# Kernel tuning notes

Measured on AMD Instinct MI355X. Metric: run time of the kernel, lower is better.

## Reference

```python
import jax, jax.numpy as jnp
import numpy as np

N, E, H, ED, TD = 10000, 320000, 128, 64, 32

def _lin(x, w, b):
    return x @ w + b

def _ln(x, g, b, eps=1e-5):
    m = jnp.mean(x, axis=-1, keepdims=True)
    v = jnp.var(x, axis=-1, keepdims=True)
    return (x - m) * jax.lax.rsqrt(v + eps) * g + b

def _mlp(x, w1, b1, g, bt, w2, b2):
    y = jax.nn.silu(_ln(_lin(x, w1, b1), g, bt))
    return _lin(y, w2, b2)

def setup_inputs() -> dict:
    key = jax.random.key(0)
    ks = jax.random.split(key, 32)
    s = 0.02
    nrm = lambda k, shp: jax.random.normal(k, shp, jnp.float32) * s
    d = {}
    d['h'] = jax.random.normal(ks[0], (N, H), jnp.float32)
    d['edge_attr'] = jax.random.normal(ks[1], (E, ED), jnp.float32)
    d['edge_time_emb'] = jax.random.normal(ks[2], (E, TD), jnp.float32)
    d['edge_index'] = jax.random.randint(ks[3], (2, E), 0, N)
    # edge_emb + edge_norm
    d['w_ee'] = nrm(ks[4], (ED + TD, ED)); d['b_ee'] = jnp.zeros((ED,), jnp.float32)
    d['g_en'] = jnp.ones((ED + TD,), jnp.float32); d['bt_en'] = jnp.zeros((ED + TD,), jnp.float32)
    # node_linear / bond_linear
    d['w_nl'] = nrm(ks[5], (H, H)); d['b_nl'] = jnp.zeros((H,), jnp.float32)
    d['w_bl'] = nrm(ks[6], (ED, H)); d['b_bl'] = jnp.zeros((H,), jnp.float32)
    # bond_linear_left/right, node_linear_left/right
    d['w_bll'] = nrm(ks[7], (ED, H)); d['b_bll'] = jnp.zeros((H,), jnp.float32)
    d['w_blr'] = nrm(ks[8], (ED, H)); d['b_blr'] = jnp.zeros((H,), jnp.float32)
    d['w_nll'] = nrm(ks[9], (H, H)); d['b_nll'] = jnp.zeros((H,), jnp.float32)
    d['w_nlr'] = nrm(ks[10], (H, H)); d['b_nlr'] = jnp.zeros((H,), jnp.float32)
    # left / right MLPs: Linear(2H,H), LayerNorm(H), SiLU, Linear(H,H)
    d['mlpl_w1'] = nrm(ks[11], (2 * H, H)); d['mlpl_b1'] = jnp.zeros((H,), jnp.float32)
    d['mlpl_g'] = jnp.ones((H,), jnp.float32); d['mlpl_bt'] = jnp.zeros((H,), jnp.float32)
    d['mlpl_w2'] = nrm(ks[12], (H, H)); d['mlpl_b2'] = jnp.zeros((H,), jnp.float32)
    d['mlpr_w1'] = nrm(ks[13], (2 * H, H)); d['mlpr_b1'] = jnp.zeros((H,), jnp.float32)
    d['mlpr_g'] = jnp.ones((H,), jnp.float32); d['mlpr_bt'] = jnp.zeros((H,), jnp.float32)
    d['mlpr_w2'] = nrm(ks[14], (H, H)); d['mlpr_b2'] = jnp.zeros((H,), jnp.float32)
    # layer_norm(3H) + bond_out: Linear(3H,H), SiLU, Linear(H,ED)
    d['g_ln'] = jnp.ones((3 * H,), jnp.float32); d['bt_ln'] = jnp.zeros((3 * H,), jnp.float32)
    d['w_o1'] = nrm(ks[15], (3 * H, H)); d['b_o1'] = jnp.zeros((H,), jnp.float32)
    d['w_o2'] = nrm(ks[16], (H, ED)); d['b_o2'] = jnp.zeros((ED,), jnp.float32)
    return d

def reference(h, edge_attr, edge_time_emb, edge_index,
              w_ee, b_ee, g_en, bt_en, w_nl, b_nl, w_bl, b_bl,
              w_bll, b_bll, w_blr, b_blr, w_nll, b_nll, w_nlr, b_nlr,
              mlpl_w1, mlpl_b1, mlpl_g, mlpl_bt, mlpl_w2, mlpl_b2,
              mlpr_w1, mlpr_b1, mlpr_g, mlpr_bt, mlpr_w2, mlpr_b2,
              g_ln, bt_ln, w_o1, b_o1, w_o2, b_o2):
    src, dst = edge_index[0], edge_index[1]
    n = h.shape[0]
    # edge_attr = edge_emb(edge_norm(cat([edge_attr, edge_time_emb])))
    ea = _lin(_ln(jnp.concatenate([edge_attr, edge_time_emb], axis=-1), g_en, bt_en), w_ee, b_ee)
    # node linears applied per-node then gathered (same math as gather-then-linear)
    x_i = _lin(h, w_nll, b_nll)[src]            # [E, H]
    x_j = _lin(h, w_nlr, b_nlr)[dst]            # [E, H]
    edge_i = _lin(ea, w_bll, b_bll)             # [E, H]
    edge_j = _lin(ea, w_blr, b_blr)             # [E, H]
    inter_i = _mlp(jnp.concatenate([edge_i, x_i], axis=-1), mlpl_w1, mlpl_b1, mlpl_g, mlpl_bt, mlpl_w2, mlpl_b2)
    inter_j = _mlp(jnp.concatenate([edge_j, x_j], axis=-1), mlpr_w1, mlpr_b1, mlpr_g, mlpr_bt, mlpr_w2, mlpr_b2)
    # scatter_sum to nodes, then regather on the same index
    inter_i = jax.ops.segment_sum(inter_i, src, num_segments=n)[src]
    inter_j = jax.ops.segment_sum(inter_j, dst, num_segments=n)[dst]
    h_node = _lin(h, w_nl, b_nl)
    h_bond = jnp.concatenate([inter_i + inter_j, h_node[src] + h_node[dst], _lin(ea, w_bl, b_bl)], axis=-1)  # [E, 3H]
    h_bond = _ln(h_bond, g_ln, bt_ln)
    out = _lin(jax.nn.silu(_lin(h_bond, w_o1, b_o1)), w_o2, b_o2)  # [E, ED]
    return out
```

## Files before the change

kernel.cpp:

```cpp
#include <hip/hip_runtime.h>
#include <math.h>


using u16 = unsigned short;
using u32 = unsigned int;
typedef __attribute__((ext_vector_type(8))) short  short8;
typedef __attribute__((ext_vector_type(4))) float  f32x4;
typedef __attribute__((ext_vector_type(4))) u32    uint4v;
typedef __attribute__((ext_vector_type(2))) u32    uint2v;

constexpr int NN = 10000;
constexpr int EE = 320000;
constexpr int MAXDEG = 96;

__device__ __forceinline__ float b2f(u16 v) {
  return __builtin_bit_cast(float, (u32)v << 16);
}
__device__ __forceinline__ float b2f_lo(u32 v) {
  return __builtin_bit_cast(float, v << 16);
}
__device__ __forceinline__ float b2f_hi(u32 v) {
  return __builtin_bit_cast(float, v & 0xffff0000u);
}
__device__ __forceinline__ u32 cvtpk(float lo, float hi) {
  u32 r;
  asm("v_cvt_pk_bf16_f32 %0, %1, %2" : "=v"(r) : "v"(lo), "v"(hi));
  return r;
}
__device__ __forceinline__ u16 f2b(float f) {
  return (u16)cvtpk(f, f);
}
__device__ __forceinline__ uint2v pack4(f32x4 v) {
  uint2v r;
  r.x = cvtpk(v[0], v[1]);
  r.y = cvtpk(v[2], v[3]);
  return r;
}
__device__ __forceinline__ u32 addpk(u32 a, u32 b) {
  return cvtpk(b2f_lo(a) + b2f_lo(b), b2f_hi(a) + b2f_hi(b));
}
__device__ __forceinline__ float silu_f(float v) {
  return v * __builtin_amdgcn_rcpf(1.f + __expf(-v));
}

struct Params {
  const void* h; const void* edge_attr; const void* te;
  const int* eidx;
  const int* flag;
  const u16 *b_ee, *g_en, *bt_en;
  const u16 *b_nl, *b_bl, *b_bll, *b_blr, *b_nll, *b_nlr;
  const u16 *l_b1, *l_g, *l_bt, *l_b2;
  const u16 *r_b1, *r_g, *r_bt, *r_b2;
  const u16 *g_ln, *bt_ln, *b_o1, *b_o2;
  const u16 *w_eeT, *w_blT, *w_bllT, *w_blrT, *w_nlT, *w_nllT, *w_nlrT;
  const u16 *l_w1T, *l_w2T, *r_w1T, *r_w2T, *o1T, *o2T;
  u16 *a_nll, *a_nlr, *h_node, *ea_ws;
  u32 *cnt0, *cnt1, *elist0, *elist1;
  u16 *accb_i, *accb_j;
  float *accf_i, *accf_j;
  u16 *inter0, *inter1;
  int amode;
  void *out;
};

__global__ __launch_bounds__(256) void k_sniff(const u16* p, int* flag)
{
  __shared__ int c;
  if (threadIdx.x == 0) c = 0;
  __syncthreads();
  u16 v = p[threadIdx.x * 2];
  int e = (v >> 7) & 0xff;
  if (e >= 100 && e <= 140) atomicAdd(&c, 1);
  __syncthreads();
  if (threadIdx.x == 0) *flag = (c >= 200) ? 1 : 0;
}

template<int K, int CT, int RT>
__device__ __forceinline__ void wave_gemm(const u16* A, int SA,
                                          const u16* __restrict__ BT,
                                          f32x4 (&acc)[RT][CT], int n0)
{
  const int lane = threadIdx.x & 63;
  const int quad = lane >> 4, l16 = lane & 15;
  constexpr int NKT = K / 32;
  short8 b[CT], bn[CT], a[RT], an[RT];
  const int k0 = quad * 8;
#pragma unroll
  for (int c = 0; c < CT; ++c)
    b[c] = *(const short8*)(BT + (size_t)(n0 + c * 16 + l16) * K + k0);
#pragma unroll
  for (int rt = 0; rt < RT; ++rt)
    a[rt] = *(const short8*)(A + (rt * 16 + l16) * SA + k0);
#pragma unroll
  for (int kt = 0; kt < NKT; ++kt) {
    if (kt + 1 < NKT) {
      const int k1 = (kt + 1) * 32 + quad * 8;
#pragma unroll
      for (int c = 0; c < CT; ++c)
        bn[c] = *(const short8*)(BT + (size_t)(n0 + c * 16 + l16) * K + k1);
#pragma unroll
      for (int rt = 0; rt < RT; ++rt)
        an[rt] = *(const short8*)(A + (rt * 16 + l16) * SA + k1);
    }
#pragma unroll
    for (int rt = 0; rt < RT; ++rt)
#pragma unroll
      for (int c = 0; c < CT; ++c)
        acc[rt][c] = __builtin_amdgcn_mfma_f32_16x16x32_bf16(a[rt], b[c], acc[rt][c], 0, 0, 0);
    if (kt + 1 < NKT) {
#pragma unroll
      for (int c = 0; c < CT; ++c) b[c] = bn[c];
#pragma unroll
      for (int rt = 0; rt < RT; ++rt) a[rt] = an[rt];
    }
  }
}

template<int CT, int RT, bool SILU>
__device__ __forceinline__ void epi_lds(f32x4 (&acc)[RT][CT], u16* O, int SO,
                                        int outc0, const u16* __restrict__ bias,
                                        int biasc0)
{
  const int lane = threadIdx.x & 63;
  const int quad = lane >> 4, l16 = lane & 15;
#pragma unroll
  for (int c = 0; c < CT; ++c) {
    float bv = b2f(bias[biasc0 + c * 16 + l16]);
#pragma unroll
    for (int rt = 0; rt < RT; ++rt) {
#pragma unroll
      for (int r = 0; r < 4; ++r) {
        float v = acc[rt][c][r] + bv;
        if (SILU) v = silu_f(v);
        O[(rt * 16 + quad * 4 + r) * SO + outc0 + c * 16 + l16] = f2b(v);
      }
    }
  }
}

template<int D, int ROWS, bool SILU>
__device__ __forceinline__ void ln_rows(u16* buf, int S,
                                        const u16* __restrict__ g,
                                        const u16* __restrict__ bt, float* red)
{
  constexpr int P = 256 / ROWS;
  constexpr int C = D / P;
  constexpr int NV = C / 8;
  const int t = threadIdx.x;
  const int row = t / P, p = t % P;
  u16* r = buf + row * S + p * C;
  uint4v vv[NV];
  float s = 0.f, ss = 0.f;
#pragma unroll
  for (int n = 0; n < NV; ++n) {
    vv[n] = *(const uint4v*)(r + n * 8);
#pragma unroll
    for (int q = 0; q < 4; ++q) {
      float lo = b2f_lo(vv[n][q]), hi = b2f_hi(vv[n][q]);
      s += lo + hi;
      ss += lo * lo + hi * hi;
    }
  }
  red[row * 2 * P + p] = s;
  red[row * 2 * P + P + p] = ss;
  __syncthreads();
  float S1 = 0.f, S2 = 0.f;
#pragma unroll
  for (int q = 0; q < P / 4; ++q) {
    f32x4 x = *(const f32x4*)&red[row * 2 * P + q * 4];
    f32x4 y = *(const f32x4*)&red[row * 2 * P + P + q * 4];
    S1 += x[0] + x[1] + x[2] + x[3];
    S2 += y[0] + y[1] + y[2] + y[3];
  }
  const float mean = S1 / (float)D;
  const float var  = S2 / (float)D - mean * mean;
  const float rstd = rsqrtf(var + 1e-5f);
#pragma unroll
  for (int n = 0; n < NV; ++n) {
    uint4v gv = *(const uint4v*)(g + p * C + n * 8);
    uint4v bv = *(const uint4v*)(bt + p * C + n * 8);
    uint4v ov;
#pragma unroll
    for (int q = 0; q < 4; ++q) {
      float lo = (b2f_lo(vv[n][q]) - mean) * rstd * b2f_lo(gv[q]) + b2f_lo(bv[q]);
      float hi = (b2f_hi(vv[n][q]) - mean) * rstd * b2f_hi(gv[q]) + b2f_hi(bv[q]);
      if (SILU) { lo = silu_f(lo); hi = silu_f(hi); }
      ov[q] = cvtpk(lo, hi);
    }
    *(uint4v*)(r + n * 8) = ov;
  }
  __syncthreads();
}

struct TDesc { const void* s; u16* d; int K; int N; };
struct TArgs { TDesc t[34]; const int* flag; };

__global__ __launch_bounds__(256) void k_transpose(TArgs a)
{
  const int flag = *a.flag;
  TDesc dsc = a.t[blockIdx.y];
  const int total = dsc.K * dsc.N;
  for (int i = blockIdx.x * 256 + threadIdx.x; i < total; i += gridDim.x * 256) {
    int n = i / dsc.K;
    int k = i - n * dsc.K;
    size_t si = (size_t)k * dsc.N + n;
    dsc.d[i] = flag ? ((const u16*)dsc.s)[si] : f2b(((const float*)dsc.s)[si]);
  }
}

__global__ __launch_bounds__(256) void k_hist(const int* eidx, u32* cnt0,
                                              u32* elist0, u32* cnt1, u32* elist1)
{
  int e = blockIdx.x * 256 + threadIdx.x;
  if (e >= EE) return;
  int n0 = eidx[e];
  u32 p0 = atomicAdd(&cnt0[n0], 1u);
  if (p0 < MAXDEG) elist0[(size_t)n0 * MAXDEG + p0] = (u32)e;
  int n1 = eidx[EE + e];
  u32 p1 = atomicAdd(&cnt1[n1], 1u);
  if (p1 < MAXDEG) elist1[(size_t)n1 * MAXDEG + p1] = (u32)e;
}

__global__ __launch_bounds__(256) void k_node(Params a)
{
  __shared__ __align__(16) u16 hs[64 * 136];
  const int tid = threadIdx.x, w = tid >> 6;
  const int n0 = blockIdx.x * 64;
  const int flag = *a.flag;
  if (flag) {
    for (int c = tid; c < 1024; c += 256) {
      int row = c >> 4, cc = c & 15;
      int node = n0 + row;
      uint4v v = {};
      if (node < NN) v = *(const uint4v*)((const u16*)a.h + (size_t)node * 128 + cc * 8);
      *(uint4v*)&hs[row * 136 + cc * 8] = v;
    }
  } else {
    for (int c = tid; c < 2048; c += 256) {
      int row = c >> 5, cc = c & 31;
      int node = n0 + row;
      uint2v pk = {};
      if (node < NN) {
        f32x4 fv = *(const f32x4*)((const float*)a.h + (size_t)node * 128 + cc * 4);
        pk = pack4(fv);
      }
      *(uint2v*)&hs[row * 136 + cc * 4] = pk;
    }
  }
  __syncthreads();
  const u16* wT[3] = { a.w_nllT, a.w_nlrT, a.w_nlT };
  const u16* bs[3] = { a.b_nll, a.b_nlr, a.b_nl };
  u16* os[3] = { a.a_nll, a.a_nlr, a.h_node };
  const int lane = tid & 63, quad = lane >> 4, l16 = lane & 15;
#pragma unroll 1
  for (int m = 0; m < 3; ++m) {
    f32x4 acc[4][2] = {};
    wave_gemm<128, 2, 4>(hs, 136, wT[m], acc, w * 32);
#pragma unroll
    for (int c = 0; c < 2; ++c) {
      int col = w * 32 + c * 16 + l16;
      float bv = b2f(bs[m][col]);
#pragma unroll
      for (int rt = 0; rt < 4; ++rt) {
#pragma unroll
        for (int r = 0; r < 4; ++r) {
          int node = n0 + rt * 16 + quad * 4 + r;
          if (node < NN) os[m][(size_t)node * 128 + col] = f2b(acc[rt][c][r] + bv);
        }
      }
    }
  }
}

__global__ __launch_bounds__(256) void k_ea(Params a)
{
  __shared__ __align__(16) u16 u[64 * 104];
  __shared__ __align__(16) u16 eas[64 * 72];
  __shared__ float red[512];
  const int tid = threadIdx.x, w = tid >> 6;
  const int e0 = blockIdx.x * 64;
  const int flag = *a.flag;
  if (flag) {
    for (int c = tid; c < 512; c += 256) {
      int row = c >> 3, cc = c & 7;
      *(uint4v*)&u[row * 104 + cc * 8] =
          *(const uint4v*)((const u16*)a.edge_attr + (size_t)(e0 + row) * 64 + cc * 8);
    }
    {
      int row = tid >> 2, cc = tid & 3;
      *(uint4v*)&u[row * 104 + 64 + cc * 8] =
          *(const uint4v*)((const u16*)a.te + (size_t)(e0 + row) * 32 + cc * 8);
    }
  } else {
    for (int c = tid; c < 1024; c += 256) {
      int row = c >> 4, cc = c & 15;
      f32x4 fv = *(const f32x4*)((const float*)a.edge_attr + (size_t)(e0 + row) * 64 + cc * 4);
      *(uint2v*)&u[row * 104 + cc * 4] = pack4(fv);
    }
    for (int c = tid; c < 512; c += 256) {
      int row = c >> 3, cc = c & 7;
      f32x4 fv = *(const f32x4*)((const float*)a.te + (size_t)(e0 + row) * 32 + cc * 4);
      *(uint2v*)&u[row * 104 + 64 + cc * 4] = pack4(fv);
    }
  }
  __syncthreads();
  ln_rows<96, 64, false>(u, 104, a.g_en, a.bt_en, red);
  {
    f32x4 acc[4][1] = {};
    wave_gemm<96, 1, 4>(u, 104, a.w_eeT, acc, w * 16);
    epi_lds<1, 4, false>(acc, eas, 72, w * 16, a.b_ee, w * 16);
  }
  __syncthreads();
  for (int c = tid; c < 512; c += 256) {
    int row = c >> 3, cc = c & 7;
    *(uint4v*)(a.ea_ws + (size_t)(e0 + row) * 64 + cc * 8) =
        *(const uint4v*)&eas[row * 72 + cc * 8];
  }
}

template<bool ATOMIC>
__global__ __launch_bounds__(256, 4) void k_mlp(
    const u16* __restrict__ ea_ws, const int* __restrict__ eidx_side,
    const u16* __restrict__ an, const u16* __restrict__ wbT,
    const u16* __restrict__ bb, const u16* __restrict__ w1T,
    const u16* __restrict__ b1, const u16* __restrict__ gg,
    const u16* __restrict__ bt, const u16* __restrict__ w2T,
    const u16* __restrict__ b2, u16* __restrict__ inter,
    float* __restrict__ accf)
{
  __shared__ __align__(16) u16 u[64 * 264];
  __shared__ float red[512];
  __shared__ int sidx[64];
  const int tid = threadIdx.x, w = tid >> 6;
  const int e0 = blockIdx.x * 64;
  const int lane = tid & 63, quad = lane >> 4, l16 = lane & 15;

  if (tid < 64) sidx[tid] = eidx_side[e0 + tid];
  __syncthreads();
  for (int c = tid; c < 1024; c += 256) {
    int row = c >> 4, cc = c & 15;
    *(uint4v*)&u[row * 264 + 128 + cc * 8] =
        *(const uint4v*)(an + (size_t)sidx[row] * 128 + cc * 8);
  }
  {
    f32x4 acc[4][2] = {};
    wave_gemm<64, 2, 4>(ea_ws + (size_t)e0 * 64, 64, wbT, acc, w * 32);
    epi_lds<2, 4, false>(acc, u, 264, w * 32, bb, w * 32);
  }
  __syncthreads();
  {
    f32x4 acc[4][2] = {};
    wave_gemm<256, 2, 4>(u, 264, w1T, acc, w * 32);
    __syncthreads();
    epi_lds<2, 4, false>(acc, u, 264, w * 32, b1, w * 32);
  }
  __syncthreads();
  ln_rows<128, 64, true>(u, 264, gg, bt, red);
  {
    f32x4 acc[4][2] = {};
    wave_gemm<128, 2, 4>(u, 264, w2T, acc, w * 32);
    if (ATOMIC) {
#pragma unroll
      for (int c = 0; c < 2; ++c) {
        int col = w * 32 + c * 16 + l16;
        float bias = b2f(b2[col]);
#pragma unroll
        for (int rt = 0; rt < 4; ++rt)
#pragma unroll
          for (int r = 0; r < 4; ++r) {
            int row = rt * 16 + quad * 4 + r;
            unsafeAtomicAdd(accf + (size_t)sidx[row] * 128 + col,
                            acc[rt][c][r] + bias);
          }
      }
    } else {
      epi_lds<2, 4, false>(acc, u, 264, 128 + w * 32, b2, w * 32);
      __syncthreads();
      for (int c = tid; c < 1024; c += 256) {
        int row = c >> 4, cc = c & 15;
        *(uint4v*)(inter + (size_t)(e0 + row) * 128 + cc * 8) =
            *(const uint4v*)&u[row * 264 + 128 + cc * 8];
      }
    }
  }
}

__global__ __launch_bounds__(256) void k_nodesum(const u16* __restrict__ inter,
                                                 const u32* __restrict__ cnt,
                                                 const u32* __restrict__ elist,
                                                 u16* __restrict__ accb)
{
  const int wv = (blockIdx.x * 256 + threadIdx.x) >> 6;
  const int lane = threadIdx.x & 63;
  if (wv >= NN) return;
  u32 deg = cnt[wv];
  if (deg > MAXDEG) deg = MAXDEG;
  const u32* el = elist + (size_t)wv * MAXDEG;
  float s0 = 0.f, s1 = 0.f;
  u32 d = 0;
  for (; d + 4 <= deg; d += 4) {
    uint4v ev = *(const uint4v*)(el + d);
    u32 v0 = *(const u32*)(inter + (size_t)ev[0] * 128 + lane * 2);
    u32 v1 = *(const u32*)(inter + (size_t)ev[1] * 128 + lane * 2);
    u32 v2 = *(const u32*)(inter + (size_t)ev[2] * 128 + lane * 2);
    u32 v3 = *(const u32*)(inter + (size_t)ev[3] * 128 + lane * 2);
    s0 += b2f_lo(v0) + b2f_lo(v1) + b2f_lo(v2) + b2f_lo(v3);
    s1 += b2f_hi(v0) + b2f_hi(v1) + b2f_hi(v2) + b2f_hi(v3);
  }
  for (; d < deg; ++d) {
    u32 e = el[d];
    u32 v = *(const u32*)(inter + (size_t)e * 128 + lane * 2);
    s0 += b2f_lo(v);
    s1 += b2f_hi(v);
  }
  *(u32*)(accb + (size_t)wv * 128 + lane * 2) = cvtpk(s0, s1);
}

__global__ __launch_bounds__(256, 4) void k_stage2(Params a)
{
  __shared__ __align__(16) u16 bond[32 * 392];
  __shared__ float red[512];
  __shared__ int sidx[2][32];
  const int tid = threadIdx.x, w = tid >> 6;
  const int e0 = blockIdx.x * 32;
  const int flag = *a.flag;
  const int lane = tid & 63, quad = lane >> 4, l16 = lane & 15;

  if (tid < 64) {
    int side = tid >> 5, i = tid & 31;
    sidx[side][i] = a.eidx[(size_t)side * EE + e0 + i];
  }
  __syncthreads();
  if (a.amode) {
    for (int c = tid; c < 512; c += 256) {
      int row = c >> 4, cc = c & 15;
      uint4v vi = *(const uint4v*)(a.accb_i + (size_t)sidx[0][row] * 128 + cc * 8);
      uint4v vj = *(const uint4v*)(a.accb_j + (size_t)sidx[1][row] * 128 + cc * 8);
      uint4v ov;
#pragma unroll
      for (int q = 0; q < 4; ++q) ov[q] = addpk(vi[q], vj[q]);
      *(uint4v*)&bond[row * 392 + cc * 8] = ov;
    }
  } else {
    for (int c = tid; c < 1024; c += 256) {
      int row = c >> 5, cc = c & 31;
      f32x4 vi = *(const f32x4*)(a.accf_i + (size_t)sidx[0][row] * 128 + cc * 4);
      f32x4 vj = *(const f32x4*)(a.accf_j + (size_t)sidx[1][row] * 128 + cc * 4);
      f32x4 sm = vi + vj;
      *(uint2v*)&bond[row * 392 + cc * 4] = pack4(sm);
    }
  }
  for (int c = tid; c < 512; c += 256) {
    int row = c >> 4, cc = c & 15;
    uint4v hs = *(const uint4v*)(a.h_node + (size_t)sidx[0][row] * 128 + cc * 8);
    uint4v hd = *(const uint4v*)(a.h_node + (size_t)sidx[1][row] * 128 + cc * 8);
    uint4v ov;
#pragma unroll
    for (int q = 0; q < 4; ++q) ov[q] = addpk(hs[q], hd[q]);
    *(uint4v*)&bond[row * 392 + 128 + cc * 8] = ov;
  }
  {
    f32x4 acc[2][2] = {};
    wave_gemm<64, 2, 2>(a.ea_ws + (size_t)e0 * 64, 64, a.w_blT, acc, w * 32);
    epi_lds<2, 2, false>(acc, bond, 392, 256 + w * 32, a.b_bl, w * 32);
  }
  __syncthreads();
  ln_rows<384, 32, false>(bond, 392, a.g_ln, a.bt_ln, red);
  {
    f32x4 acc[2][2] = {};
    wave_gemm<384, 2, 2>(bond, 392, a.o1T, acc, w * 32);
    __syncthreads();
    epi_lds<2, 2, true>(acc, bond, 392, w * 32, a.b_o1, w * 32);
  }
  __syncthreads();
  {
    f32x4 acc[2][1] = {};
    wave_gemm<128, 1, 2>(bond, 392, a.o2T, acc, w * 16);
    if (flag) {
      epi_lds<1, 2, false>(acc, bond, 392, 128 + w * 16, a.b_o2, w * 16);
      __syncthreads();
      for (int c = tid; c < 256; c += 256) {
        int row = c >> 3, cc = c & 7;
        *(uint4v*)((u16*)a.out + (size_t)(e0 + row) * 64 + cc * 8) =
            *(const uint4v*)&bond[row * 392 + 128 + cc * 8];
      }
    } else {
      float bvv = b2f(a.b_o2[w * 16 + l16]);
#pragma unroll
      for (int rt = 0; rt < 2; ++rt)
#pragma unroll
        for (int r = 0; r < 4; ++r) {
          int row = rt * 16 + quad * 4 + r;
          ((float*)((char*)bond + (size_t)row * 784 + 272))[w * 16 + l16] =
              acc[rt][0][r] + bvv;
        }
      __syncthreads();
      for (int c = tid; c < 512; c += 256) {
        int row = c >> 4, cc = c & 15;
        f32x4 v = *(const f32x4*)((char*)bond + (size_t)row * 784 + 272 + cc * 16);
        *(f32x4*)((float*)a.out + (size_t)(e0 + row) * 64 + cc * 4) = v;
      }
    }
  }
}

extern "C" void kernel_launch(void* const* d_in, const int* in_sizes, int n_in,
                              void* d_out, int out_size, void* d_ws, size_t ws_size,
                              hipStream_t stream)
{
  char* ws = (char*)d_ws;

  const size_t O_EET  = 0;
  const size_t O_BLT  = 12288;
  const size_t O_BLLT = O_BLT  + 16384;
  const size_t O_BLRT = O_BLLT + 16384;
  const size_t O_NLT  = O_BLRT + 16384;
  const size_t O_NLLT = O_NLT  + 32768;
  const size_t O_NLRT = O_NLLT + 32768;
  const size_t O_LW1T = O_NLRT + 32768;
  const size_t O_LW2T = O_LW1T + 65536;
  const size_t O_RW1T = O_LW2T + 32768;
  const size_t O_RW2T = O_RW1T + 65536;
  const size_t O_O1T  = O_RW2T + 32768;
  const size_t O_O2T  = O_O1T  + 98304;
  const size_t PRM    = O_O2T  + 16384;
  const size_t FLAG   = PRM + 6016;
  const size_t A_NLL  = PRM + 6144;
  const size_t A_NLR  = A_NLL + 2560000;
  const size_t H_NODE = A_NLR + 2560000;
  const size_t EA     = H_NODE + 2560000;
  const size_t TAIL   = EA + 40960000;
  const size_t ACCF_I = TAIL;
  const size_t ACCF_J = TAIL + 5120000;
  const size_t NEED_ATOM = TAIL + 10240000;
  const size_t CNT0   = TAIL;
  const size_t CNT1   = TAIL + 40960;
  const size_t EL0    = TAIL + 81920;
  const size_t EL1    = EL0 + 3840000;
  const size_t ACCB_I = EL1 + 3840000;
  const size_t ACCB_J = ACCB_I + 2560000;
  const size_t INTER0 = ACCB_J + 2560000;
  const size_t NEED_CSR = INTER0 + 81920000;
  if (ws_size < NEED_ATOM) return;
  const int amode = (ws_size >= NEED_CSR) ? 1 : 0;

  const size_t pOff[21] = { 0, 128, 320, 512, 768, 1024, 1280, 1536, 1792,
                            2048, 2304, 2560, 2816, 3072, 3328, 3584, 3840,
                            4096, 4864, 5632, 5888 };
  const int   pIdx[21] = { 5, 6, 7, 9, 11, 13, 15, 17, 19,
                           21, 22, 23, 25, 27, 28, 29, 31,
                           32, 33, 35, 37 };
  const int   pLen[21] = { 64, 96, 96, 128, 128, 128, 128, 128, 128,
                           128, 128, 128, 128, 128, 128, 128, 128,
                           384, 384, 128, 64 };
  auto P = [&](int slot) { return (const u16*)(ws + PRM + pOff[slot]); };

  Params a;
  a.h = d_in[0]; a.edge_attr = d_in[1]; a.te = d_in[2];
  a.eidx = (const int*)d_in[3];
  a.flag = (const int*)(ws + FLAG);
  a.b_ee = P(0); a.g_en = P(1); a.bt_en = P(2);
  a.b_nl = P(3); a.b_bl = P(4); a.b_bll = P(5); a.b_blr = P(6);
  a.b_nll = P(7); a.b_nlr = P(8);
  a.l_b1 = P(9); a.l_g = P(10); a.l_bt = P(11); a.l_b2 = P(12);
  a.r_b1 = P(13); a.r_g = P(14); a.r_bt = P(15); a.r_b2 = P(16);
  a.g_ln = P(17); a.bt_ln = P(18); a.b_o1 = P(19); a.b_o2 = P(20);
  a.w_eeT = (const u16*)(ws + O_EET);   a.w_blT  = (const u16*)(ws + O_BLT);
  a.w_bllT = (const u16*)(ws + O_BLLT); a.w_blrT = (const u16*)(ws + O_BLRT);
  a.w_nlT = (const u16*)(ws + O_NLT);   a.w_nllT = (const u16*)(ws + O_NLLT);
  a.w_nlrT = (const u16*)(ws + O_NLRT);
  a.l_w1T = (const u16*)(ws + O_LW1T);  a.l_w2T = (const u16*)(ws + O_LW2T);
  a.r_w1T = (const u16*)(ws + O_RW1T);  a.r_w2T = (const u16*)(ws + O_RW2T);
  a.o1T = (const u16*)(ws + O_O1T);     a.o2T = (const u16*)(ws + O_O2T);
  a.a_nll = (u16*)(ws + A_NLL); a.a_nlr = (u16*)(ws + A_NLR);
  a.h_node = (u16*)(ws + H_NODE); a.ea_ws = (u16*)(ws + EA);
  a.cnt0 = (u32*)(ws + CNT0); a.cnt1 = (u32*)(ws + CNT1);
  a.elist0 = (u32*)(ws + EL0); a.elist1 = (u32*)(ws + EL1);
  a.accb_i = (u16*)(ws + ACCB_I); a.accb_j = (u16*)(ws + ACCB_J);
  a.accf_i = (float*)(ws + ACCF_I); a.accf_j = (float*)(ws + ACCF_J);
  a.inter0 = (u16*)(ws + INTER0); a.inter1 = (u16*)(ws + INTER0);
  a.amode = amode;
  a.out = d_out;

  TArgs ta;
  ta.flag = (const int*)(ws + FLAG);
  ta.t[0]  = { d_in[4],  (u16*)(ws + O_EET),  96, 64 };
  ta.t[1]  = { d_in[10], (u16*)(ws + O_BLT),  64, 128 };
  ta.t[2]  = { d_in[12], (u16*)(ws + O_BLLT), 64, 128 };
  ta.t[3]  = { d_in[14], (u16*)(ws + O_BLRT), 64, 128 };
  ta.t[4]  = { d_in[8],  (u16*)(ws + O_NLT),  128, 128 };
  ta.t[5]  = { d_in[16], (u16*)(ws + O_NLLT), 128, 128 };
  ta.t[6]  = { d_in[18], (u16*)(ws + O_NLRT), 128, 128 };
  ta.t[7]  = { d_in[20], (u16*)(ws + O_LW1T), 256, 128 };
  ta.t[8]  = { d_in[24], (u16*)(ws + O_LW2T), 128, 128 };
  ta.t[9]  = { d_in[26], (u16*)(ws + O_RW1T), 256, 128 };
  ta.t[10] = { d_in[30], (u16*)(ws + O_RW2T), 128, 128 };
  ta.t[11] = { d_in[34], (u16*)(ws + O_O1T),  384, 128 };
  ta.t[12] = { d_in[36], (u16*)(ws + O_O2T),  128, 64 };
  for (int s = 0; s < 21; ++s)
    ta.t[13 + s] = { d_in[pIdx[s]], (u16*)(ws + PRM + pOff[s]), 1, pLen[s] };

  k_sniff<<<1, 256, 0, stream>>>((const u16*)d_in[1], (int*)(ws + FLAG));
  if (amode) hipMemsetAsync(ws + CNT0, 0, 81920, stream);
  else       hipMemsetAsync(ws + ACCF_I, 0, 10240000, stream);
  k_transpose<<<dim3(16, 34), 256, 0, stream>>>(ta);
  if (amode)
    k_hist<<<(EE + 255) / 256, 256, 0, stream>>>(a.eidx, a.cnt0, a.elist0, a.cnt1, a.elist1);
  k_node<<<(NN + 63) / 64, 256, 0, stream>>>(a);
  k_ea<<<EE / 64, 256, 0, stream>>>(a);

  if (amode) {
    k_mlp<false><<<EE / 64, 256, 0, stream>>>(a.ea_ws, a.eidx, a.a_nll, a.w_bllT,
        a.b_bll, a.l_w1T, a.l_b1, a.l_g, a.l_bt, a.l_w2T, a.l_b2, a.inter0, nullptr);
    k_nodesum<<<(NN * 64 + 255) / 256, 256, 0, stream>>>(a.inter0, a.cnt0, a.elist0, a.accb_i);
    k_mlp<false><<<EE / 64, 256, 0, stream>>>(a.ea_ws, a.eidx + EE, a.a_nlr, a.w_blrT,
        a.b_blr, a.r_w1T, a.r_b1, a.r_g, a.r_bt, a.r_w2T, a.r_b2, a.inter1, nullptr);
    k_nodesum<<<(NN * 64 + 255) / 256, 256, 0, stream>>>(a.inter1, a.cnt1, a.elist1, a.accb_j);
  } else {
    k_mlp<true><<<EE / 64, 256, 0, stream>>>(a.ea_ws, a.eidx, a.a_nll, a.w_bllT,
        a.b_bll, a.l_w1T, a.l_b1, a.l_g, a.l_bt, a.l_w2T, a.l_b2, nullptr, a.accf_i);
    k_mlp<true><<<EE / 64, 256, 0, stream>>>(a.ea_ws, a.eidx + EE, a.a_nlr, a.w_blrT,
        a.b_blr, a.r_w1T, a.r_b1, a.r_g, a.r_bt, a.r_w2T, a.r_b2, nullptr, a.accf_j);
  }
  k_stage2<<<EE / 32, 256, 0, stream>>>(a);
}
```

Measured before the change: 753.9 us.

## Interleave node sums with h_node in one table and use nontemporal streaming accesses

Node-level summed interactions for the src side and h_node now share one interleaved 256-wide table, so k_stage2 in atomic-free mode reads one contiguous 512-byte row per src node instead of two separate 256-byte gathers. The two gather loops merge into one loop over 32 chunks per row. Streaming loads and stores of inputs, inter buffers and outputs use nontemporal hints to reduce cache pollution. Risks: nontemporal loads on the gathered inter rows in k_nodesum may lose L2 reuse, and the fallback path must index the new table stride correctly.

```diff
diff --git a/kernel.cpp b/kernel.cpp
--- a/kernel.cpp
+++ b/kernel.cpp
@@ -42,6 +42,10 @@
 __device__ __forceinline__ float silu_f(float v) {
   return v * __builtin_amdgcn_rcpf(1.f + __expf(-v));
 }
+template<typename T>
+__device__ __forceinline__ T ntld(const T* p) { return __builtin_nontemporal_load(p); }
+template<typename T>
+__device__ __forceinline__ void ntst(T* p, T v) { __builtin_nontemporal_store(v, p); }
 
 struct Params {
   const void* h; const void* edge_attr; const void* te;
@@ -54,9 +58,9 @@
   const u16 *g_ln, *bt_ln, *b_o1, *b_o2;
   const u16 *w_eeT, *w_blT, *w_bllT, *w_blrT, *w_nlT, *w_nllT, *w_nlrT;
   const u16 *l_w1T, *l_w2T, *r_w1T, *r_w2T, *o1T, *o2T;
-  u16 *a_nll, *a_nlr, *h_node, *ea_ws;
+  u16 *a_nll, *a_nlr, *tbl_i, *ea_ws;
   u32 *cnt0, *cnt1, *elist0, *elist1;
-  u16 *accb_i, *accb_j;
+  u16 *accb_j;
   float *accf_i, *accf_j;
   u16 *inter0, *inter1;
   int amode;
@@ -232,7 +236,7 @@
       int row = c >> 4, cc = c & 15;
       int node = n0 + row;
       uint4v v = {};
-      if (node < NN) v = *(const uint4v*)((const u16*)a.h + (size_t)node * 128 + cc * 8);
+      if (node < NN) v = ntld((const uint4v*)((const u16*)a.h + (size_t)node * 128 + cc * 8));
       *(uint4v*)&hs[row * 136 + cc * 8] = v;
     }
   } else {
@@ -241,7 +245,7 @@
       int node = n0 + row;
       uint2v pk = {};
       if (node < NN) {
-        f32x4 fv = *(const f32x4*)((const float*)a.h + (size_t)node * 128 + cc * 4);
+        f32x4 fv = ntld((const f32x4*)((const float*)a.h + (size_t)node * 128 + cc * 4));
         pk = pack4(fv);
       }
       *(uint2v*)&hs[row * 136 + cc * 4] = pk;
@@ -250,7 +254,8 @@
   __syncthreads();
   const u16* wT[3] = { a.w_nllT, a.w_nlrT, a.w_nlT };
   const u16* bs[3] = { a.b_nll, a.b_nlr, a.b_nl };
-  u16* os[3] = { a.a_nll, a.a_nlr, a.h_node };
+  u16* os[3] = { a.a_nll, a.a_nlr, a.tbl_i + 128 };
+  const int st[3] = { 128, 128, 256 };
   const int lane = tid & 63, quad = lane >> 4, l16 = lane & 15;
 #pragma unroll 1
   for (int m = 0; m < 3; ++m) {
@@ -265,7 +270,7 @@
 #pragma unroll
         for (int r = 0; r < 4; ++r) {
           int node = n0 + rt * 16 + quad * 4 + r;
-          if (node < NN) os[m][(size_t)node * 128 + col] = f2b(acc[rt][c][r] + bv);
+          if (node < NN) os[m][(size_t)node * st[m] + col] = f2b(acc[rt][c][r] + bv);
         }
       }
     }
@@ -284,22 +289,22 @@
     for (int c = tid; c < 512; c += 256) {
       int row = c >> 3, cc = c & 7;
       *(uint4v*)&u[row * 104 + cc * 8] =
-          *(const uint4v*)((const u16*)a.edge_attr + (size_t)(e0 + row) * 64 + cc * 8);
+          ntld((const uint4v*)((const u16*)a.edge_attr + (size_t)(e0 + row) * 64 + cc * 8));
     }
     {
       int row = tid >> 2, cc = tid & 3;
       *(uint4v*)&u[row * 104 + 64 + cc * 8] =
-          *(const uint4v*)((const u16*)a.te + (size_t)(e0 + row) * 32 + cc * 8);
+          ntld((const uint4v*)((const u16*)a.te + (size_t)(e0 + row) * 32 + cc * 8));
     }
   } else {
     for (int c = tid; c < 1024; c += 256) {
       int row = c >> 4, cc = c & 15;
-      f32x4 fv = *(const f32x4*)((const float*)a.edge_attr + (size_t)(e0 + row) * 64 + cc * 4);
+      f32x4 fv = ntld((const f32x4*)((const float*)a.edge_attr + (size_t)(e0 + row) * 64 + cc * 4));
       *(uint2v*)&u[row * 104 + cc * 4] = pack4(fv);
     }
     for (int c = tid; c < 512; c += 256) {
       int row = c >> 3, cc = c & 7;
-      f32x4 fv = *(const f32x4*)((const float*)a.te + (size_t)(e0 + row) * 32 + cc * 4);
+      f32x4 fv = ntld((const f32x4*)((const float*)a.te + (size_t)(e0 + row) * 32 + cc * 4));
       *(uint2v*)&u[row * 104 + 64 + cc * 4] = pack4(fv);
     }
   }
@@ -378,8 +383,8 @@
       __syncthreads();
       for (int c = tid; c < 1024; c += 256) {
         int row = c >> 4, cc = c & 15;
-        *(uint4v*)(inter + (size_t)(e0 + row) * 128 + cc * 8) =
-            *(const uint4v*)&u[row * 264 + 128 + cc * 8];
+        ntst((uint4v*)(inter + (size_t)(e0 + row) * 128 + cc * 8),
+             *(const uint4v*)&u[row * 264 + 128 + cc * 8]);
       }
     }
   }
@@ -388,7 +393,7 @@
 __global__ __launch_bounds__(256) void k_nodesum(const u16* __restrict__ inter,
                                                  const u32* __restrict__ cnt,
                                                  const u32* __restrict__ elist,
-                                                 u16* __restrict__ accb)
+                                                 u16* __restrict__ dst, int dstride)
 {
   const int wv = (blockIdx.x * 256 + threadIdx.x) >> 6;
   const int lane = threadIdx.x & 63;
@@ -399,21 +404,21 @@
   float s0 = 0.f, s1 = 0.f;
   u32 d = 0;
   for (; d + 4 <= deg; d += 4) {
-    uint4v ev = *(const uint4v*)(el + d);
-    u32 v0 = *(const u32*)(inter + (size_t)ev[0] * 128 + lane * 2);
-    u32 v1 = *(const u32*)(inter + (size_t)ev[1] * 128 + lane * 2);
-    u32 v2 = *(const u32*)(inter + (size_t)ev[2] * 128 + lane * 2);
-    u32 v3 = *(const u32*)(inter + (size_t)ev[3] * 128 + lane * 2);
+    uint4v ev = ntld((const uint4v*)(el + d));
+    u32 v0 = ntld((const u32*)(inter + (size_t)ev[0] * 128 + lane * 2));
+    u32 v1 = ntld((const u32*)(inter + (size_t)ev[1] * 128 + lane * 2));
+    u32 v2 = ntld((const u32*)(inter + (size_t)ev[2] * 128 + lane * 2));
+    u32 v3 = ntld((const u32*)(inter + (size_t)ev[3] * 128 + lane * 2));
     s0 += b2f_lo(v0) + b2f_lo(v1) + b2f_lo(v2) + b2f_lo(v3);
     s1 += b2f_hi(v0) + b2f_hi(v1) + b2f_hi(v2) + b2f_hi(v3);
   }
   for (; d < deg; ++d) {
     u32 e = el[d];
-    u32 v = *(const u32*)(inter + (size_t)e * 128 + lane * 2);
+    u32 v = ntld((const u32*)(inter + (size_t)e * 128 + lane * 2));
     s0 += b2f_lo(v);
     s1 += b2f_hi(v);
   }
-  *(u32*)(accb + (size_t)wv * 128 + lane * 2) = cvtpk(s0, s1);
+  *(u32*)(dst + (size_t)wv * dstride + lane * 2) = cvtpk(s0, s1);
 }
 
 __global__ __launch_bounds__(256, 4) void k_stage2(Params a)
@@ -432,13 +437,17 @@
   }
   __syncthreads();
   if (a.amode) {
-    for (int c = tid; c < 512; c += 256) {
-      int row = c >> 4, cc = c & 15;
-      uint4v vi = *(const uint4v*)(a.accb_i + (size_t)sidx[0][row] * 128 + cc * 8);
-      uint4v vj = *(const uint4v*)(a.accb_j + (size_t)sidx[1][row] * 128 + cc * 8);
+    for (int c = tid; c < 1024; c += 256) {
+      int row = c >> 5, cc = c & 31;
+      const u16* ps = a.tbl_i + (size_t)sidx[0][row] * 256 + cc * 8;
+      const u16* pp = (cc < 16)
+          ? a.accb_j + (size_t)sidx[1][row] * 128 + cc * 8
+          : a.tbl_i + (size_t)sidx[1][row] * 256 + cc * 8;
+      uint4v vs = *(const uint4v*)ps;
+      uint4v vp = *(const uint4v*)pp;
       uint4v ov;
 #pragma unroll
-      for (int q = 0; q < 4; ++q) ov[q] = addpk(vi[q], vj[q]);
+      for (int q = 0; q < 4; ++q) ov[q] = addpk(vs[q], vp[q]);
       *(uint4v*)&bond[row * 392 + cc * 8] = ov;
     }
   } else {
@@ -449,15 +458,15 @@
       f32x4 sm = vi + vj;
       *(uint2v*)&bond[row * 392 + cc * 4] = pack4(sm);
     }
-  }
-  for (int c = tid; c < 512; c += 256) {
-    int row = c >> 4, cc = c & 15;
-    uint4v hs = *(const uint4v*)(a.h_node + (size_t)sidx[0][row] * 128 + cc * 8);
-    uint4v hd = *(const uint4v*)(a.h_node + (size_t)sidx[1][row] * 128 + cc * 8);
-    uint4v ov;
-#pragma unroll
-    for (int q = 0; q < 4; ++q) ov[q] = addpk(hs[q], hd[q]);
-    *(uint4v*)&bond[row * 392 + 128 + cc * 8] = ov;
+    for (int c = tid; c < 512; c += 256) {
+      int row = c >> 4, cc = c & 15;
+      uint4v hs = *(const uint4v*)(a.tbl_i + (size_t)sidx[0][row] * 256 + 128 + cc * 8);
+      uint4v hd = *(const uint4v*)(a.tbl_i + (size_t)sidx[1][row] * 256 + 128 + cc * 8);
+      uint4v ov;
+#pragma unroll
+      for (int q = 0; q < 4; ++q) ov[q] = addpk(hs[q], hd[q]);
+      *(uint4v*)&bond[row * 392 + 128 + cc * 8] = ov;
+    }
   }
   {
     f32x4 acc[2][2] = {};
@@ -481,8 +490,8 @@
       __syncthreads();
       for (int c = tid; c < 256; c += 256) {
         int row = c >> 3, cc = c & 7;
-        *(uint4v*)((u16*)a.out + (size_t)(e0 + row) * 64 + cc * 8) =
-            *(const uint4v*)&bond[row * 392 + 128 + cc * 8];
+        ntst((uint4v*)((u16*)a.out + (size_t)(e0 + row) * 64 + cc * 8),
+             *(const uint4v*)&bond[row * 392 + 128 + cc * 8]);
       }
     } else {
       float bvv = b2f(a.b_o2[w * 16 + l16]);
@@ -498,7 +507,7 @@
       for (int c = tid; c < 512; c += 256) {
         int row = c >> 4, cc = c & 15;
         f32x4 v = *(const f32x4*)((char*)bond + (size_t)row * 784 + 272 + cc * 16);
-        *(f32x4*)((float*)a.out + (size_t)(e0 + row) * 64 + cc * 4) = v;
+        ntst((f32x4*)((float*)a.out + (size_t)(e0 + row) * 64 + cc * 4), v);
       }
     }
   }
@@ -527,8 +536,8 @@
   const size_t FLAG   = PRM + 6016;
   const size_t A_NLL  = PRM + 6144;
   const size_t A_NLR  = A_NLL + 2560000;
-  const size_t H_NODE = A_NLR + 2560000;
-  const size_t EA     = H_NODE + 2560000;
+  const size_t TBL_I  = A_NLR + 2560000;
+  const size_t EA     = TBL_I + 5120000;
   const size_t TAIL   = EA + 40960000;
   const size_t ACCF_I = TAIL;
   const size_t ACCF_J = TAIL + 5120000;
@@ -537,8 +546,7 @@
   const size_t CNT1   = TAIL + 40960;
   const size_t EL0    = TAIL + 81920;
   const size_t EL1    = EL0 + 3840000;
-  const size_t ACCB_I = EL1 + 3840000;
-  const size_t ACCB_J = ACCB_I + 2560000;
+  const size_t ACCB_J = EL1 + 3840000;
   const size_t INTER0 = ACCB_J + 2560000;
   const size_t NEED_CSR = INTER0 + 81920000;
   if (ws_size < NEED_ATOM) return;
@@ -573,10 +581,10 @@
   a.r_w1T = (const u16*)(ws + O_RW1T);  a.r_w2T = (const u16*)(ws + O_RW2T);
   a.o1T = (const u16*)(ws + O_O1T);     a.o2T = (const u16*)(ws + O_O2T);
   a.a_nll = (u16*)(ws + A_NLL); a.a_nlr = (u16*)(ws + A_NLR);
-  a.h_node = (u16*)(ws + H_NODE); a.ea_ws = (u16*)(ws + EA);
+  a.tbl_i = (u16*)(ws + TBL_I); a.ea_ws = (u16*)(ws + EA);
   a.cnt0 = (u32*)(ws + CNT0); a.cnt1 = (u32*)(ws + CNT1);
   a.elist0 = (u32*)(ws + EL0); a.elist1 = (u32*)(ws + EL1);
-  a.accb_i = (u16*)(ws + ACCB_I); a.accb_j = (u16*)(ws + ACCB_J);
+  a.accb_j = (u16*)(ws + ACCB_J);
   a.accf_i = (float*)(ws + ACCF_I); a.accf_j = (float*)(ws + ACCF_J);
   a.inter0 = (u16*)(ws + INTER0); a.inter1 = (u16*)(ws + INTER0);
   a.amode = amode;
@@ -612,10 +620,12 @@
   if (amode) {
     k_mlp<false><<<EE / 64, 256, 0, stream>>>(a.ea_ws, a.eidx, a.a_nll, a.w_bllT,
         a.b_bll, a.l_w1T, a.l_b1, a.l_g, a.l_bt, a.l_w2T, a.l_b2, a.inter0, nullptr);
-    k_nodesum<<<(NN * 64 + 255) / 256, 256, 0, stream>>>(a.inter0, a.cnt0, a.elist0, a.accb_i);
+    k_nodesum<<<(NN * 64 + 255) / 256, 256, 0, stream>>>(a.inter0, a.cnt0, a.elist0,
+        a.tbl_i, 256);
     k_mlp<false><<<EE / 64, 256, 0, stream>>>(a.ea_ws, a.eidx + EE, a.a_nlr, a.w_blrT,
         a.b_blr, a.r_w1T, a.r_b1, a.r_g, a.r_bt, a.r_w2T, a.r_b2, a.inter1, nullptr);
-    k_nodesum<<<(NN * 64 + 255) / 256, 256, 0, stream>>>(a.inter1, a.cnt1, a.elist1, a.accb_j);
+    k_nodesum<<<(NN * 64 + 255) / 256, 256, 0, stream>>>(a.inter1, a.cnt1, a.elist1,
+        a.accb_j, 128);
   } else {
     k_mlp<true><<<EE / 64, 256, 0, stream>>>(a.ea_ws, a.eidx, a.a_nll, a.w_bllT,
         a.b_bll, a.l_w1T, a.l_b1, a.l_g, a.l_bt, a.l_w2T, a.l_b2, nullptr, a.accf_i);
```

Result: no change. 755.0 us (+0.2%).
